# Performance work log

Hardware: AMD Instinct MI355X
Metric: run time of the kernel (lower is better)

## Reference

```python
import jax, jax.numpy as jnp
import numpy as np

N_NODES = 50000
IN_CH = 128
N_EDGES = 800000
ADD_CONST = 0.5


def setup_inputs() -> dict:
    key = jax.random.key(0)
    k1, k2, k3, k4, k5 = jax.random.split(key, 5)
    x = jax.random.normal(k1, (N_NODES, IN_CH), dtype=jnp.float32)
    edge_index = jax.random.randint(k2, (2, N_EDGES), 0, N_NODES, dtype=jnp.int32)
    edge_weight = jax.random.uniform(k3, (N_EDGES,), dtype=jnp.float32)
    # Linear(2*C -> 1): split into source/target halves (mathematically identical
    # to Linear on concat([x[row], x[col]])). Xavier-uniform-ish scale.
    lim = float(np.sqrt(6.0 / (2 * IN_CH + 1)))
    w_src = jax.random.uniform(k4, (IN_CH,), minval=-lim, maxval=lim, dtype=jnp.float32)
    w_dst = jax.random.uniform(k5, (IN_CH,), minval=-lim, maxval=lim, dtype=jnp.float32)
    b = jnp.zeros((), dtype=jnp.float32)
    return {"x": x, "w_src": w_src, "w_dst": w_dst, "b": b,
            "edge_index": edge_index, "edge_weight": edge_weight}


def _normalize_edge_score(score, row, num_nodes):
    """Per-source-node softmax over strictly-positive scores, +0.5; nodes with
    no positive incident edge keep raw scores (faithful to torch loop)."""
    pos = score > 0
    has_pos = jax.ops.segment_max(pos.astype(jnp.int32), row, num_segments=num_nodes) > 0
    neg_big = jnp.asarray(jnp.finfo(score.dtype).min, score.dtype)
    smax = jax.ops.segment_max(jnp.where(pos, score, neg_big), row, num_segments=num_nodes)
    safe_max = jnp.where(has_pos, smax, 0.0)
    exp_s = jnp.where(pos, jnp.exp(score - safe_max[row]), 0.0)
    denom = jax.ops.segment_sum(exp_s, row, num_segments=num_nodes)
    denom = jnp.where(denom > 0, denom, 1.0)
    soft = jnp.where(pos, exp_s / denom[row] + ADD_CONST, 0.0)
    return jnp.where(has_pos[row], soft, score)


def reference(x, w_src, w_dst, b, edge_index, edge_weight):
    N = x.shape[0]
    row, col = edge_index[0], edge_index[1]

    # Edge score: Linear on concat([x[row], x[col]]) == per-node projections gathered.
    score = (x @ w_src)[row] + (x @ w_dst)[col] + b          # [E]
    norm = _normalize_edge_score(score, row, N)              # [E]

    # Greedy contraction in descending score order. Because the torch loop skips
    # any edge whose endpoint cluster already has size > 1, this is exactly a
    # greedy maximal matching: carry only a per-node 'matched' bitmask.
    perm = jnp.argsort(-norm)
    r_s, c_s, s_s = row[perm], col[perm], norm[perm]

    def step(matched, uv):
        u, v = uv
        ok = (u != v) & ~matched[u] & ~matched[v]
        matched = matched.at[u].set(matched[u] | ok)
        matched = matched.at[v].set(matched[v] | ok)
        return matched, ok

    _, sel = jax.lax.scan(step, jnp.zeros((N,), dtype=bool), (r_s, c_s))  # sel: [E]

    # cluster[v] = u for each selected edge (u, v); everything else identity.
    drop_v = jnp.where(sel, c_s, N)   # out-of-range indices are dropped
    drop_u = jnp.where(sel, r_s, N)
    cluster = jnp.arange(N, dtype=jnp.int32).at[drop_v].set(r_s, mode='drop')
    s_rep = jnp.ones((N,), x.dtype).at[drop_u].set(s_s, mode='drop')       # score of merging edge at rep u
    partner = jnp.arange(N, dtype=jnp.int32).at[drop_u].set(c_s, mode='drop')
    rep_sel = jnp.zeros((N,), bool).at[drop_u].set(True, mode='drop')

    # torch: merged_x[u] = (x[u] + x[v]) * s ; merged_x[v] stays x[v];
    # new_x = index_add by cluster  =>  rep u gets (x[u]+x[v])*s + x[v].
    sum_x = jax.ops.segment_sum(x, cluster, num_segments=N)               # [N, C]
    new_x = sum_x * s_rep[:, None] + jnp.where(rep_sel[:, None], x[partner], 0.0)

    counts = jax.ops.segment_sum(jnp.ones((N,), jnp.int32), cluster, num_segments=N)
    is_rep = counts > 0          # rows of new_x that correspond to surviving clusters

    # Remap edges to cluster representatives; self-loops masked out.
    new_row = cluster[row]
    new_col = cluster[col]
    edge_valid = new_row != new_col

    return new_x, cluster, is_rep, new_row, new_col, edge_valid, edge_weight
```

## Files before the change

kernel.cpp:

```cpp
#include <hip/hip_runtime.h>
#include <cmath>

#define IN_CH 128
#define NBUCK 256
#define LNMAX 196
#define PLW(p) __hip_atomic_load((p), __ATOMIC_RELAXED, __HIP_MEMORY_SCOPE_WORKGROUP)

typedef unsigned long long ull;
typedef ull  ull2 __attribute__((ext_vector_type(2)));
typedef float f4  __attribute__((ext_vector_type(4)));

__device__ __forceinline__ ull make_key(float norm, int e) {
    unsigned int b = __float_as_uint(norm);
    unsigned int asc = (b & 0x80000000u) ? ~b : (b | 0x80000000u);
    unsigned int desc = ~asc;
    return (((ull)desc) << 32) | (unsigned int)e;
}

__global__ void proj_kernel(const float* __restrict__ x, const float* __restrict__ w_src,
                            const float* __restrict__ w_dst, float* __restrict__ p,
                            float* __restrict__ q,
                            ull* __restrict__ wsuit,
                            int* __restrict__ cluster, int* __restrict__ partner,
                            float* __restrict__ s_rep, int* __restrict__ bump,
                            int* __restrict__ btail, int N) {
    int gtid = blockIdx.x * blockDim.x + threadIdx.x;
    if (gtid == 0) *bump = 0;
    if (gtid < NBUCK) btail[gtid] = 0;
    if (gtid < N) {
        wsuit[gtid]    = ~0ULL;
        cluster[gtid]  = gtid;
        partner[gtid]  = gtid;
        s_rep[gtid]    = 1.0f;
    }
    int wave = gtid >> 6;
    int lane = threadIdx.x & 63;
    if (wave >= N) return;
    float2 xv = ((const float2*)(x + (size_t)wave * IN_CH))[lane];
    float2 ws = ((const float2*)w_src)[lane];
    float2 wd = ((const float2*)w_dst)[lane];
    double ap = (double)xv.x * (double)ws.x + (double)xv.y * (double)ws.y;
    double aq = (double)xv.x * (double)wd.x + (double)xv.y * (double)wd.y;
    #pragma unroll
    for (int off = 32; off > 0; off >>= 1) {
        ap += __shfl_down(ap, off);
        aq += __shfl_down(aq, off);
    }
    if (lane == 0) { p[wave] = (float)ap; q[wave] = (float)aq; }
}

__global__ void score_kernel(const int* __restrict__ row, const int* __restrict__ col,
                             const float* __restrict__ p, const float* __restrict__ q,
                             const float* __restrict__ bptr, float* __restrict__ score,
                             int2* __restrict__ rc, int* __restrict__ btail,
                             unsigned int* __restrict__ bucket, int bcap, int E) {
    __shared__ int cnt[NBUCK];
    __shared__ int gbase[NBUCK];
    int e = blockIdx.x * blockDim.x + threadIdx.x;
    if (threadIdx.x < NBUCK) cnt[threadIdx.x] = 0;
    __syncthreads();
    bool inb = e < E;
    int u = 0, v = 0, l1 = -1, l2 = -1, h1 = 0, h2 = 0;
    unsigned int selfbit = 0;
    if (inb) {
        u = row[e]; v = col[e];
        rc[e] = make_int2(u, v);
        float s = p[u] + q[v] + bptr[0];
        score[e] = s;
        selfbit = (u == v) ? (1u << 30) : 0u;
        h1 = u & (NBUCK - 1); l1 = atomicAdd(&cnt[h1], 1);
        if (u != v) {
            h2 = v & (NBUCK - 1); l2 = atomicAdd(&cnt[h2], 1);
        }
    }
    __syncthreads();
    if (threadIdx.x < NBUCK) gbase[threadIdx.x] = atomicAdd(&btail[threadIdx.x], cnt[threadIdx.x]);
    __syncthreads();
    if (l1 >= 0) bucket[(size_t)h1 * bcap + gbase[h1] + l1] =
        (unsigned int)e | ((unsigned int)(u >> 8) << 21) | selfbit;
    if (l2 >= 0) bucket[(size_t)h2 * bcap + gbase[h2] + l2] =
        (unsigned int)e | (1u << 20) | ((unsigned int)(v >> 8) << 21);
}

__global__ void slot_kernel(unsigned int* __restrict__ bucket, const int* __restrict__ btail,
                            int bcap, const float* __restrict__ score,
                            unsigned int* __restrict__ node_max, double* __restrict__ denom,
                            int* __restrict__ bump, int2* __restrict__ seg, int N) {
    __shared__ int hist[LNMAX];
    __shared__ unsigned int maxv[LNMAX];
    __shared__ double dden[LNMAX];
    __shared__ int scan[256];
    __shared__ int basesh;
    int b = blockIdx.x;
    int t = threadIdx.x;
    for (int i = t; i < LNMAX; i += blockDim.x) {
        hist[i] = 0; maxv[i] = 0u; dden[i] = 0.0;
    }
    __syncthreads();
    int n = btail[b];
    unsigned int* bk = bucket + (size_t)b * bcap;
    for (int i = t; i < n; i += blockDim.x) {
        unsigned int ent = bk[i];
        if (!(ent & (1u << 20))) {
            int e = (int)(ent & 0xfffffu);
            float s = score[e];
            if (s > 0.0f) {
                int ln = (int)((ent >> 21) & 0x1ffu);
                atomicMax(&maxv[ln], __float_as_uint(s));
            }
        }
    }
    __syncthreads();
    for (int i = t; i < n; i += blockDim.x) {
        unsigned int ent = bk[i];
        int ln = (int)((ent >> 21) & 0x1ffu);
        if (!(ent & (1u << 20))) {
            unsigned int mb = maxv[ln];
            int e = (int)(ent & 0xfffffu);
            float s = score[e];
            if (mb != 0u && s > 0.0f) {
                float m = __uint_as_float(mb);
                float ev = (float)exp((double)(s - m));
                atomicAdd(&dden[ln], (double)ev);
            }
        }
        if (ent & (1u << 30)) {
            bk[i] = 0xFFFFFFFFu;
        } else {
            int slot = atomicAdd(&hist[ln], 1);
            bk[i] = (ent & 0x1fffffu) | ((unsigned int)slot << 21);
        }
    }
    __syncthreads();
    if (t < 256) {
        int node = (t << 8) | b;
        int d = (t < LNMAX && node < N) ? hist[t] : 0;
        scan[t] = (d + 3) & ~3;
    }
    __syncthreads();
    #pragma unroll
    for (int off = 1; off < 256; off <<= 1) {
        int add = (t < 256 && t >= off) ? scan[t - off] : 0;
        __syncthreads();
        if (t < 256) scan[t] += add;
        __syncthreads();
    }
    if (t == 255) basesh = atomicAdd(bump, scan[255]);
    __syncthreads();
    if (t < LNMAX) {
        int node = (t << 8) | b;
        if (node < N) {
            int d  = hist[t];
            int pd = (d + 3) & ~3;
            int lo = basesh + scan[t] - pd;
            seg[node]      = make_int2(lo, lo + d);
            node_max[node] = maxv[t];
            denom[node]    = dden[t];
        }
    }
}

__global__ void norm_key_kernel(const int* __restrict__ row, const float* __restrict__ score,
                                const unsigned int* __restrict__ node_max,
                                const double* __restrict__ denom, float* __restrict__ norm,
                                ull* __restrict__ keyn, int E) {
    int e = blockIdx.x * blockDim.x + threadIdx.x;
    if (e >= E) return;
    int u = row[e];
    unsigned int mb = node_max[u];
    float nv;
    if (mb != 0u) {
        float s = score[e];
        if (s > 0.0f) {
            float m = __uint_as_float(mb);
            float ev = (float)exp((double)(s - m));
            float d = (float)denom[u];
            nv = ev / d + 0.5f;
        } else {
            nv = 0.0f;
        }
    } else {
        nv = score[e];
    }
    norm[e] = nv;
    keyn[e] = make_key(nv, e);
}

__global__ void csr_scatter_kernel(const unsigned int* __restrict__ bucket,
                                   const int* __restrict__ btail, int bcap,
                                   const ull* __restrict__ keyn, const int2* __restrict__ rc,
                                   const int2* __restrict__ seg,
                                   ull2* __restrict__ adj, int bpx) {
    int xcd = blockIdx.x & 7;
    int sub = blockIdx.x >> 3;
    for (int bb = 0; bb < NBUCK / 8; ++bb) {
        int b = xcd + (bb << 3);
        int n = btail[b];
        const unsigned int* bk = bucket + (size_t)b * bcap;
        for (int i = sub * blockDim.x + threadIdx.x; i < n; i += bpx * blockDim.x) {
            unsigned int ent = bk[i];
            if (ent == 0xFFFFFFFFu) continue;
            int e    = (int)(ent & 0xfffffu);
            int side = (int)((ent >> 20) & 1u);
            int slot = (int)(ent >> 21);
            int2 pr = rc[e];
            int dst = side ? pr.y : pr.x;
            int nb  = side ? pr.x : pr.y;
            ull2 w; w.x = keyn[e]; w.y = (ull)nb;
            adj[seg[dst].x + slot] = w;
        }
    }
}

__global__ void suitor_kernel(const int2* __restrict__ seg,
                              const ull2* __restrict__ adj,
                              const int2* __restrict__ rc,
                              ull* __restrict__ ws, int N) {
    int lg   = threadIdx.x >> 5;
    int b    = blockIdx.x;
    int grp  = ((((b >> 3) << 3) + lg) << 3) | (b & 7);
    int lane = threadIdx.x & 31;
    if (grp >= N) return;
    int cur = grp;
    int2 lohi;
    ull excl = 0ULL;
    ull lk = ~0ULL;
    int lv = -1;
    bool reload = true;
    for (int guard = 0; guard < 1000000; ++guard) {
        if (reload) {
            lohi = seg[cur];
            excl = 0ULL;
            lk = ~0ULL; lv = -1;
            for (int i = lohi.x + lane; i < lohi.y; i += 32) {
                ull2 ent = adj[i];
                ull k = ent.x;
                if (k < lk) {
                    int v = (int)ent.y;
                    if (k < PLW(&ws[v])) { lk = k; lv = v; }
                }
            }
            reload = false;
        } else if (lk != ~0ULL && lk <= excl) {
            lk = ~0ULL; lv = -1;
            for (int i = lohi.x + lane; i < lohi.y; i += 32) {
                ull2 ent = adj[i];
                ull k = ent.x;
                if (k > excl && k < lk) {
                    int v = (int)ent.y;
                    if (k < PLW(&ws[v])) { lk = k; lv = v; }
                }
            }
        }
        ull bk = lk; int bv = lv;
        #pragma unroll
        for (int off = 16; off > 0; off >>= 1) {
            ull ok = __shfl_xor(bk, off, 32);
            int ov = __shfl_xor(bv, off, 32);
            if (ok < bk) { bk = ok; bv = ov; }
        }
        if (bk == ~0ULL) break;
        ull old;
        if (lane == 0) old = atomicMin(&ws[bv], bk);
        old = __shfl(old, 0, 32);
        if (old <= bk) {
            excl = bk;
            continue;
        }
        if (old == ~0ULL) break;
        int e = (int)(old & 0xffffffffu);
        int2 pr = rc[e];
        cur = pr.x ^ pr.y ^ bv;
        reload = true;
    }
}

__global__ void extract_kernel(const int2* __restrict__ rc, const float* __restrict__ norm,
                               const ull* __restrict__ ws,
                               int* __restrict__ cluster, int* __restrict__ partner,
                               float* __restrict__ s_rep, int N) {
    int w = blockIdx.x * blockDim.x + threadIdx.x;
    if (w >= N) return;
    ull k = ws[w];
    if (k == ~0ULL) return;
    int e = (int)(k & 0xffffffffu);
    int2 pr = rc[e];
    int a = pr.x, b = pr.y;
    if (w != a) return;
    if (ws[b] == k) {
        cluster[b] = a;
        partner[a] = b;
        s_rep[a]   = norm[e];
    }
}

__global__ void out_kernel(const float* __restrict__ x, const int* __restrict__ cluster,
                           const int* __restrict__ partner, const float* __restrict__ s_rep,
                           const int* __restrict__ row, const int* __restrict__ col,
                           const float* __restrict__ w,
                           float* __restrict__ out_newx, float* __restrict__ out_cluster,
                           float* __restrict__ out_isrep, float* __restrict__ out_nrow,
                           float* __restrict__ out_ncol, float* __restrict__ out_valid,
                           float* __restrict__ out_w, int N, int E, int NB1) {
    if ((int)blockIdx.x < NB1) {
        int t = blockIdx.x * blockDim.x + threadIdx.x;
        if (t >= N * (IN_CH / 4)) return;
        int n = t >> 5;
        int c = (t & 31) * 4;
        int cl = cluster[n];
        if ((t & 31) == 0) {
            out_cluster[n] = (float)cl;
            out_isrep[n]   = (cl == n) ? 1.0f : 0.0f;
        }
        f4 o;
        int v = partner[n];
        if (cl != n) {
            o = (f4)0.0f;
        } else if (v != n) {
            float s = s_rep[n];
            f4 xu = *(const f4*)(x + (size_t)n * IN_CH + c);
            f4 xv = *(const f4*)(x + (size_t)v * IN_CH + c);
            o = (xu + xv) * s + xv;
        } else {
            o = *(const f4*)(x + (size_t)n * IN_CH + c);
        }
        __builtin_nontemporal_store(o, (f4*)out_newx + t);
    } else {
        int e = (blockIdx.x - NB1) * blockDim.x + threadIdx.x;
        if (e >= E) return;
        int nr = cluster[row[e]];
        int nc = cluster[col[e]];
        out_nrow[e]  = (float)nr;
        out_ncol[e]  = (float)nc;
        out_valid[e] = (nr != nc) ? 1.0f : 0.0f;
        out_w[e]     = w[e];
    }
}

extern "C" void kernel_launch(void* const* d_in, const int* in_sizes, int n_in_args,
                              void* d_out, int out_size, void* d_ws, size_t ws_size,
                              hipStream_t stream) {
    const float* x     = (const float*)d_in[0];
    const float* w_src = (const float*)d_in[1];
    const float* w_dst = (const float*)d_in[2];
    const float* bptr  = (const float*)d_in[3];
    const int*   ei    = (const int*)d_in[4];
    const float* ew    = (const float*)d_in[5];
    const int N = in_sizes[0] / IN_CH;
    const int E = in_sizes[5];
    const int* row = ei;
    const int* col = ei + E;

    char* wsb = (char*)d_ws;
    size_t off = 0;
    auto alloc = [&](size_t bytes) -> void* {
        off = (off + 255) & ~(size_t)255;
        void* ptr = wsb + off;
        off += bytes;
        return ptr;
    };
    const int bcap = E / 128 + E / 1024 + 1024;
    float*        score    = (float*)alloc((size_t)E * 4);
    float*        norm     = (float*)alloc((size_t)E * 4);
    int2*         rc       = (int2*)alloc((size_t)E * 8);
    ull*          keyn     = (ull*)alloc((size_t)E * 8);
    ull2*         adj      = (ull2*)alloc(((size_t)2 * E + 4 * N) * 16);
    unsigned int* bucket   = (unsigned int*)alloc((size_t)NBUCK * bcap * 4);
    unsigned int* node_max = (unsigned int*)alloc((size_t)N * 4);
    double*       denom    = (double*)alloc((size_t)N * 8);
    ull*          wsuit    = (ull*)alloc((size_t)N * 8);
    int2*         seg      = (int2*)alloc((size_t)N * 8);
    int*          cluster  = (int*)alloc((size_t)N * 4);
    int*          partner  = (int*)alloc((size_t)N * 4);
    float*        s_rep    = (float*)alloc((size_t)N * 4);
    float*        pbuf     = (float*)alloc((size_t)N * 4);
    float*        qbuf     = (float*)alloc((size_t)N * 4);
    int*          bump     = (int*)alloc(64);
    int*          btail    = (int*)alloc((size_t)NBUCK * 4);

    float* out       = (float*)d_out;
    float* o_newx    = out;
    float* o_cluster = out + (size_t)N * IN_CH;
    float* o_isrep   = o_cluster + N;
    float* o_nrow    = o_isrep + N;
    float* o_ncol    = o_nrow + E;
    float* o_valid   = o_ncol + E;
    float* o_w       = o_valid + E;

    const int T = 256;
    const int TS = 1024;
    hipLaunchKernelGGL(proj_kernel, dim3((N * 64 + T - 1) / T), dim3(T), 0, stream,
                       x, w_src, w_dst, pbuf, qbuf,
                       wsuit, cluster, partner, s_rep, bump, btail, N);
    hipLaunchKernelGGL(score_kernel, dim3((E + TS - 1) / TS), dim3(TS), 0, stream,
                       row, col, pbuf, qbuf, bptr, score, rc,
                       btail, bucket, bcap, E);
    hipLaunchKernelGGL(slot_kernel, dim3(NBUCK), dim3(1024), 0, stream,
                       bucket, btail, bcap, score, node_max, denom, bump, seg, N);
    hipLaunchKernelGGL(norm_key_kernel, dim3((E + T - 1) / T), dim3(T), 0, stream,
                       row, score, node_max, denom, norm, keyn, E);
    const int bpx = 80;
    hipLaunchKernelGGL(csr_scatter_kernel, dim3(8 * bpx), dim3(T), 0, stream,
                       bucket, btail, bcap, keyn, rc, seg, adj, bpx);
    const int SB = ((N + 63) / 64) * 8;
    hipLaunchKernelGGL(suitor_kernel, dim3(SB), dim3(T), 0, stream,
                       seg, adj, rc, wsuit, N);
    hipLaunchKernelGGL(extract_kernel, dim3((N + T - 1) / T), dim3(T), 0, stream,
                       rc, norm, wsuit, cluster, partner, s_rep, N);
    const int NB1 = (N * 32 + T - 1) / T;
    const int NB2 = (E + T - 1) / T;
    hipLaunchKernelGGL(out_kernel, dim3(NB1 + NB2), dim3(T), 0, stream,
                       x, cluster, partner, s_rep, row, col, ew,
                       o_newx, o_cluster, o_isrep, o_nrow, o_ncol, o_valid, o_w, N, E, NB1);
    (void)ws_size; (void)out_size; (void)n_in_args;
}
```

Baseline: 316.4 us.

## Carry score and neighbor in buckets, fuse normalization into CSR scatter

Bucket entries now carry the edge score and the neighbor/local-node index in a side array, so slot_kernel and csr_scatter no longer do random gathers of score[e], rc[e] and keyn[e]. The separate norm_key kernel is removed: the normalized score and sort key are computed inside csr_scatter, and extract_kernel recomputes the score from p/q. This cuts one launch and several E-sized random-access arrays, at the cost of wider bucket entries (12 bytes instead of 4) and duplicated exp/div work per directed edge.

```diff
diff --git a/kernel.cpp b/kernel.cpp
--- a/kernel.cpp
+++ b/kernel.cpp
@@ -4,6 +4,8 @@
 #define IN_CH 128
 #define NBUCK 256
 #define LNMAX 196
+#define SIDE_BIT (1u << 20)
+#define SELF_BIT (1u << 21)
 #define PLW(p) __hip_atomic_load((p), __ATOMIC_RELAXED, __HIP_MEMORY_SCOPE_WORKGROUP)
 
 typedef unsigned long long ull;
@@ -15,6 +17,19 @@
     unsigned int asc = (b & 0x80000000u) ? ~b : (b | 0x80000000u);
     unsigned int desc = ~asc;
     return (((ull)desc) << 32) | (unsigned int)e;
+}
+
+__device__ __forceinline__ float norm_from(float s, unsigned int mb, double den) {
+    if (mb != 0u) {
+        if (s > 0.0f) {
+            float m = __uint_as_float(mb);
+            float ev = (float)exp((double)(s - m));
+            float d = (float)den;
+            return ev / d + 0.5f;
+        }
+        return 0.0f;
+    }
+    return s;
 }
 
 __global__ void proj_kernel(const float* __restrict__ x, const float* __restrict__ w_src,
@@ -51,9 +66,10 @@
 
 __global__ void score_kernel(const int* __restrict__ row, const int* __restrict__ col,
                              const float* __restrict__ p, const float* __restrict__ q,
-                             const float* __restrict__ bptr, float* __restrict__ score,
+                             const float* __restrict__ bptr,
                              int2* __restrict__ rc, int* __restrict__ btail,
-                             unsigned int* __restrict__ bucket, int bcap, int E) {
+                             uint2* __restrict__ bucketA, float* __restrict__ bucketS,
+                             int bcap, int E) {
     __shared__ int cnt[NBUCK];
     __shared__ int gbase[NBUCK];
     int e = blockIdx.x * blockDim.x + threadIdx.x;
@@ -61,13 +77,11 @@
     __syncthreads();
     bool inb = e < E;
     int u = 0, v = 0, l1 = -1, l2 = -1, h1 = 0, h2 = 0;
-    unsigned int selfbit = 0;
+    float s = 0.0f;
     if (inb) {
         u = row[e]; v = col[e];
         rc[e] = make_int2(u, v);
-        float s = p[u] + q[v] + bptr[0];
-        score[e] = s;
-        selfbit = (u == v) ? (1u << 30) : 0u;
+        s = p[u] + q[v] + bptr[0];
         h1 = u & (NBUCK - 1); l1 = atomicAdd(&cnt[h1], 1);
         if (u != v) {
             h2 = v & (NBUCK - 1); l2 = atomicAdd(&cnt[h2], 1);
@@ -76,14 +90,22 @@
     __syncthreads();
     if (threadIdx.x < NBUCK) gbase[threadIdx.x] = atomicAdd(&btail[threadIdx.x], cnt[threadIdx.x]);
     __syncthreads();
-    if (l1 >= 0) bucket[(size_t)h1 * bcap + gbase[h1] + l1] =
-        (unsigned int)e | ((unsigned int)(u >> 8) << 21) | selfbit;
-    if (l2 >= 0) bucket[(size_t)h2 * bcap + gbase[h2] + l2] =
-        (unsigned int)e | (1u << 20) | ((unsigned int)(v >> 8) << 21);
-}
-
-__global__ void slot_kernel(unsigned int* __restrict__ bucket, const int* __restrict__ btail,
-                            int bcap, const float* __restrict__ score,
+    if (l1 >= 0) {
+        size_t idx = (size_t)h1 * bcap + gbase[h1] + l1;
+        unsigned int w0 = (unsigned int)e | ((u == v) ? SELF_BIT : 0u);
+        bucketA[idx] = make_uint2(w0, (unsigned int)v | ((unsigned int)(u >> 8) << 17));
+        bucketS[idx] = s;
+    }
+    if (l2 >= 0) {
+        size_t idx = (size_t)h2 * bcap + gbase[h2] + l2;
+        bucketA[idx] = make_uint2((unsigned int)e | SIDE_BIT,
+                                  (unsigned int)u | ((unsigned int)(v >> 8) << 17));
+        bucketS[idx] = s;
+    }
+}
+
+__global__ void slot_kernel(uint2* __restrict__ bucketA, const float* __restrict__ bucketS,
+                            const int* __restrict__ btail, int bcap,
                             unsigned int* __restrict__ node_max, double* __restrict__ denom,
                             int* __restrict__ bump, int2* __restrict__ seg, int N) {
     __shared__ int hist[LNMAX];
@@ -98,37 +120,36 @@
     }
     __syncthreads();
     int n = btail[b];
-    unsigned int* bk = bucket + (size_t)b * bcap;
+    uint2* bkA = bucketA + (size_t)b * bcap;
+    const float* bkS = bucketS + (size_t)b * bcap;
     for (int i = t; i < n; i += blockDim.x) {
-        unsigned int ent = bk[i];
-        if (!(ent & (1u << 20))) {
-            int e = (int)(ent & 0xfffffu);
-            float s = score[e];
+        uint2 en = bkA[i];
+        if (!(en.x & SIDE_BIT)) {
+            float s = bkS[i];
             if (s > 0.0f) {
-                int ln = (int)((ent >> 21) & 0x1ffu);
+                int ln = (int)((en.y >> 17) & 0x1ffu);
                 atomicMax(&maxv[ln], __float_as_uint(s));
             }
         }
     }
     __syncthreads();
     for (int i = t; i < n; i += blockDim.x) {
-        unsigned int ent = bk[i];
-        int ln = (int)((ent >> 21) & 0x1ffu);
-        if (!(ent & (1u << 20))) {
+        uint2 en = bkA[i];
+        int ln = (int)((en.y >> 17) & 0x1ffu);
+        if (!(en.x & SIDE_BIT)) {
             unsigned int mb = maxv[ln];
-            int e = (int)(ent & 0xfffffu);
-            float s = score[e];
+            float s = bkS[i];
             if (mb != 0u && s > 0.0f) {
                 float m = __uint_as_float(mb);
                 float ev = (float)exp((double)(s - m));
                 atomicAdd(&dden[ln], (double)ev);
             }
         }
-        if (ent & (1u << 30)) {
-            bk[i] = 0xFFFFFFFFu;
+        if (en.x & SELF_BIT) {
+            bkA[i].x = 0xFFFFFFFFu;
         } else {
             int slot = atomicAdd(&hist[ln], 1);
-            bk[i] = (ent & 0x1fffffu) | ((unsigned int)slot << 21);
+            bkA[i].x = (en.x & 0x1fffffu) | ((unsigned int)slot << 21);
         }
     }
     __syncthreads();
@@ -160,35 +181,11 @@
     }
 }
 
-__global__ void norm_key_kernel(const int* __restrict__ row, const float* __restrict__ score,
-                                const unsigned int* __restrict__ node_max,
-                                const double* __restrict__ denom, float* __restrict__ norm,
-                                ull* __restrict__ keyn, int E) {
-    int e = blockIdx.x * blockDim.x + threadIdx.x;
-    if (e >= E) return;
-    int u = row[e];
-    unsigned int mb = node_max[u];
-    float nv;
-    if (mb != 0u) {
-        float s = score[e];
-        if (s > 0.0f) {
-            float m = __uint_as_float(mb);
-            float ev = (float)exp((double)(s - m));
-            float d = (float)denom[u];
-            nv = ev / d + 0.5f;
-        } else {
-            nv = 0.0f;
-        }
-    } else {
-        nv = score[e];
-    }
-    norm[e] = nv;
-    keyn[e] = make_key(nv, e);
-}
-
-__global__ void csr_scatter_kernel(const unsigned int* __restrict__ bucket,
+__global__ void csr_scatter_kernel(const uint2* __restrict__ bucketA,
+                                   const float* __restrict__ bucketS,
                                    const int* __restrict__ btail, int bcap,
-                                   const ull* __restrict__ keyn, const int2* __restrict__ rc,
+                                   const unsigned int* __restrict__ node_max,
+                                   const double* __restrict__ denom,
                                    const int2* __restrict__ seg,
                                    ull2* __restrict__ adj, int bpx) {
     int xcd = blockIdx.x & 7;
@@ -196,17 +193,20 @@
     for (int bb = 0; bb < NBUCK / 8; ++bb) {
         int b = xcd + (bb << 3);
         int n = btail[b];
-        const unsigned int* bk = bucket + (size_t)b * bcap;
+        const uint2* bkA = bucketA + (size_t)b * bcap;
+        const float* bkS = bucketS + (size_t)b * bcap;
         for (int i = sub * blockDim.x + threadIdx.x; i < n; i += bpx * blockDim.x) {
-            unsigned int ent = bk[i];
-            if (ent == 0xFFFFFFFFu) continue;
-            int e    = (int)(ent & 0xfffffu);
-            int side = (int)((ent >> 20) & 1u);
-            int slot = (int)(ent >> 21);
-            int2 pr = rc[e];
-            int dst = side ? pr.y : pr.x;
-            int nb  = side ? pr.x : pr.y;
-            ull2 w; w.x = keyn[e]; w.y = (ull)nb;
+            uint2 en = bkA[i];
+            if (en.x == 0xFFFFFFFFu) continue;
+            int e    = (int)(en.x & 0xfffffu);
+            int side = (int)((en.x >> 20) & 1u);
+            int slot = (int)(en.x >> 21);
+            int nb   = (int)(en.y & 0x1ffffu);
+            int ln   = (int)((en.y >> 17) & 0x1ffu);
+            int dst  = (ln << 8) | b;
+            int u    = side ? nb : dst;
+            float nv = norm_from(bkS[i], node_max[u], denom[u]);
+            ull2 w; w.x = make_key(nv, e); w.y = (ull)nb;
             adj[seg[dst].x + slot] = w;
         }
     }
@@ -275,7 +275,11 @@
     }
 }
 
-__global__ void extract_kernel(const int2* __restrict__ rc, const float* __restrict__ norm,
+__global__ void extract_kernel(const int2* __restrict__ rc,
+                               const float* __restrict__ p, const float* __restrict__ q,
+                               const float* __restrict__ bptr,
+                               const unsigned int* __restrict__ node_max,
+                               const double* __restrict__ denom,
                                const ull* __restrict__ ws,
                                int* __restrict__ cluster, int* __restrict__ partner,
                                float* __restrict__ s_rep, int N) {
@@ -290,7 +294,8 @@
     if (ws[b] == k) {
         cluster[b] = a;
         partner[a] = b;
-        s_rep[a]   = norm[e];
+        float s = p[a] + q[b] + bptr[0];
+        s_rep[a] = norm_from(s, node_max[a], denom[a]);
     }
 }
 
@@ -360,12 +365,10 @@
         return ptr;
     };
     const int bcap = E / 128 + E / 1024 + 1024;
-    float*        score    = (float*)alloc((size_t)E * 4);
-    float*        norm     = (float*)alloc((size_t)E * 4);
     int2*         rc       = (int2*)alloc((size_t)E * 8);
-    ull*          keyn     = (ull*)alloc((size_t)E * 8);
     ull2*         adj      = (ull2*)alloc(((size_t)2 * E + 4 * N) * 16);
-    unsigned int* bucket   = (unsigned int*)alloc((size_t)NBUCK * bcap * 4);
+    uint2*        bucketA  = (uint2*)alloc((size_t)NBUCK * bcap * 8);
+    float*        bucketS  = (float*)alloc((size_t)NBUCK * bcap * 4);
     unsigned int* node_max = (unsigned int*)alloc((size_t)N * 4);
     double*       denom    = (double*)alloc((size_t)N * 8);
     ull*          wsuit    = (ull*)alloc((size_t)N * 8);
@@ -393,20 +396,19 @@
                        x, w_src, w_dst, pbuf, qbuf,
                        wsuit, cluster, partner, s_rep, bump, btail, N);
     hipLaunchKernelGGL(score_kernel, dim3((E + TS - 1) / TS), dim3(TS), 0, stream,
-                       row, col, pbuf, qbuf, bptr, score, rc,
-                       btail, bucket, bcap, E);
+                       row, col, pbuf, qbuf, bptr, rc,
+                       btail, bucketA, bucketS, bcap, E);
     hipLaunchKernelGGL(slot_kernel, dim3(NBUCK), dim3(1024), 0, stream,
-                       bucket, btail, bcap, score, node_max, denom, bump, seg, N);
-    hipLaunchKernelGGL(norm_key_kernel, dim3((E + T - 1) / T), dim3(T), 0, stream,
-                       row, score, node_max, denom, norm, keyn, E);
+                       bucketA, bucketS, btail, bcap, node_max, denom, bump, seg, N);
     const int bpx = 80;
     hipLaunchKernelGGL(csr_scatter_kernel, dim3(8 * bpx), dim3(T), 0, stream,
-                       bucket, btail, bcap, keyn, rc, seg, adj, bpx);
+                       bucketA, bucketS, btail, bcap, node_max, denom, seg, adj, bpx);
     const int SB = ((N + 63) / 64) * 8;
     hipLaunchKernelGGL(suitor_kernel, dim3(SB), dim3(T), 0, stream,
                        seg, adj, rc, wsuit, N);
     hipLaunchKernelGGL(extract_kernel, dim3((N + T - 1) / T), dim3(T), 0, stream,
-                       rc, norm, wsuit, cluster, partner, s_rep, N);
+                       rc, pbuf, qbuf, bptr, node_max, denom, wsuit,
+                       cluster, partner, s_rep, N);
     const int NB1 = (N * 32 + T - 1) / T;
     const int NB2 = (E + T - 1) / T;
     hipLaunchKernelGGL(out_kernel, dim3(NB1 + NB2), dim3(T), 0, stream,
```

Result: faster. 295.9 us (-6.5%).
